# Performance work log

Hardware: AMD Instinct MI355X
Metric: run time of the kernel (lower is better)

## Reference

```python
import jax, jax.numpy as jnp
import numpy as np

D_MODEL = 1024
D_FF = 2048
NUM_EXPERTS = 16
TOP_K = 2
CAPACITY_FACTOR = 1.25
BATCH, SEQ = 4, 2048


def setup_inputs() -> dict:
    key = jax.random.key(0)
    k0, k1, k2, k3 = jax.random.split(key, 4)
    x = jax.random.normal(k0, (BATCH, SEQ, D_MODEL), jnp.float32)
    gate_w = jax.random.normal(k1, (NUM_EXPERTS, D_MODEL), jnp.float32) / np.float32(np.sqrt(D_MODEL))
    w1 = jax.random.normal(k2, (NUM_EXPERTS, D_MODEL, D_FF), jnp.float32) / np.float32(np.sqrt(D_MODEL))
    w2 = jax.random.normal(k3, (NUM_EXPERTS, D_FF, D_MODEL), jnp.float32) / np.float32(np.sqrt(D_FF))
    return {"x": x, "gate_w": gate_w, "w1": w1, "w2": w2}


def reference(x, gate_w, w1, w2):
    B, S, d = x.shape
    T = B * S
    E, K = NUM_EXPERTS, TOP_K
    capacity = int(CAPACITY_FACTOR * T * K / E)  # static

    xf = x.reshape(T, d)                                  # [T, d]
    logits = xf @ gate_w.T                                # [T, E]
    probs = jax.nn.sigmoid(logits)
    top_vals, sel = jax.lax.top_k(probs, K)               # [T, K]
    weights = top_vals / (top_vals.sum(-1, keepdims=True) + 1e-6)

    # Capacity-based ranking: rank of each (token, slot) within its expert,
    # in flattened token-major order (matches torch cumsum over one-hot).
    flat_sel = sel.reshape(-1)                            # [T*K]
    onehot = jax.nn.one_hot(flat_sel, E, dtype=jnp.int32)
    ranks = jnp.take_along_axis(jnp.cumsum(onehot, axis=0), flat_sel[:, None], axis=1)[:, 0] - 1
    valid = ranks < capacity                              # [T*K]

    sentinel = E * capacity
    slot = jnp.where(valid, flat_sel * capacity + ranks, sentinel)

    # token-major repeat matches x_flat.unsqueeze(1).expand(-1,K,-1).reshape(-1,d)
    x_rep = jnp.repeat(xf, K, axis=0)                     # [T*K, d]
    padded = jnp.zeros((sentinel + 1, d), xf.dtype).at[slot].set(x_rep)
    padded = padded[:sentinel].reshape(E, capacity, d)    # [E, C, d]

    h = jax.nn.gelu(jnp.einsum('ecd,edf->ecf', padded, w1), approximate=False)
    out_padded = jnp.einsum('ecf,efd->ecd', h, w2).reshape(sentinel, d)

    gathered = out_padded[jnp.minimum(slot, sentinel - 1)]
    gathered = jnp.where(valid[:, None], gathered, jnp.zeros((), xf.dtype))
    out = (gathered * weights.reshape(-1)[:, None]).reshape(T, K, d).sum(axis=1)
    return out.reshape(B, S, d)
```

## Files before the change

kernel.cpp:

```cpp
#include <hip/hip_runtime.h>
#include <math.h>

#define T_TOK 8192
#define DM 1024
#define DF 2048
#define NE 16
#define TK 2
#define CAP 1280

typedef __bf16 bf16x8 __attribute__((ext_vector_type(8)));
typedef float f32x4 __attribute__((ext_vector_type(4)));

__device__ __forceinline__ unsigned short f2bf(float f) {
  unsigned int u = __float_as_uint(f);
  unsigned int r = (u + 0x7fffu + ((u >> 16) & 1u)) >> 16;
  return (unsigned short)r;
}

__device__ __forceinline__ void async_copy16(const void* g, void* l) {
  __builtin_amdgcn_global_load_lds(
      (const __attribute__((address_space(1))) void*)g,
      (__attribute__((address_space(3))) void*)l, 16, 0, 0);
}

__global__ __launch_bounds__(256) void transpose_conv_kernel(
    const float* __restrict__ in, unsigned short* __restrict__ out, int R, int Cc) {
  __shared__ unsigned short tl[64][72];
  size_t eoff = (size_t)blockIdx.z * R * Cc;
  in += eoff; out += eoff;
  int c0 = blockIdx.x * 64, r0 = blockIdx.y * 64;
  int t = threadIdx.x;
#pragma unroll
  for (int i = 0; i < 4; i++) {
    int r = (t >> 4) + i * 16;
    int c = (t & 15) * 4;
    float4 v = *(const float4*)(in + (size_t)(r0 + r) * Cc + c0 + c);
    tl[c + 0][r] = f2bf(v.x);
    tl[c + 1][r] = f2bf(v.y);
    tl[c + 2][r] = f2bf(v.z);
    tl[c + 3][r] = f2bf(v.w);
  }
  __syncthreads();
#pragma unroll
  for (int i = 0; i < 2; i++) {
    int c = (t >> 3) + i * 32;
    int r = (t & 7) * 8;
    *(int4*)(out + (size_t)(c0 + c) * R + r0 + r) = *(const int4*)&tl[c][r];
  }
}

__global__ __launch_bounds__(256) void gate_kernel(
    const float* __restrict__ x, const float* __restrict__ gw,
    int* __restrict__ sel, float* __restrict__ wts) {
  __shared__ float sgw[NE * DM];
  int tid = threadIdx.x, lane = tid & 63, wv = tid >> 6;
  for (int i = tid; i < NE * DM / 4; i += 256)
    ((float4*)sgw)[i] = ((const float4*)gw)[i];
  __syncthreads();
  int t = blockIdx.x * 4 + wv;
  const float4* xr = (const float4*)(x + (size_t)t * DM);
  float4 xv[4];
#pragma unroll
  for (int j = 0; j < 4; j++) xv[j] = xr[j * 64 + lane];
  const float4* g4 = (const float4*)sgw;
  float acc[NE];
#pragma unroll
  for (int e = 0; e < NE; e++) {
    float s = 0.f;
#pragma unroll
    for (int j = 0; j < 4; j++) {
      float4 g = g4[e * 256 + j * 64 + lane];
      s += xv[j].x * g.x + xv[j].y * g.y + xv[j].z * g.z + xv[j].w * g.w;
    }
    acc[e] = s;
  }
#pragma unroll
  for (int e = 0; e < NE; e++) {
    float v = acc[e];
#pragma unroll
    for (int off = 32; off > 0; off >>= 1) v += __shfl_xor(v, off);
    acc[e] = v;
  }
  if (lane == 0) {
    float p[NE];
#pragma unroll
    for (int e = 0; e < NE; e++) p[e] = 1.f / (1.f + expf(-acc[e]));
    int i0 = 0;
#pragma unroll
    for (int e = 1; e < NE; e++) if (p[e] > p[i0]) i0 = e;
    int i1 = (i0 == 0) ? 1 : 0;
#pragma unroll
    for (int e = 0; e < NE; e++) if (e != i0 && p[e] > p[i1]) i1 = e;
    float v0 = p[i0], v1 = p[i1], s = v0 + v1 + 1e-6f;
    sel[2 * t] = i0; sel[2 * t + 1] = i1;
    wts[2 * t] = v0 / s; wts[2 * t + 1] = v1 / s;
  }
}

__global__ __launch_bounds__(256) void scan_kernel(
    const int* __restrict__ sel, int* __restrict__ exp_tok, int* __restrict__ counts) {
  int e = blockIdx.x;
  __shared__ int wsum[4];
  int tid = threadIdx.x, lane = tid & 63, wv = tid >> 6;
  int base = 0;
  for (int p0 = 0; p0 < T_TOK * TK; p0 += 256) {
    int p = p0 + tid;
    int flag = (sel[p] == e) ? 1 : 0;
    unsigned long long b = __ballot(flag);
    int pre = __popcll(b & ((1ull << lane) - 1ull));
    if (lane == 0) wsum[wv] = __popcll(b);
    __syncthreads();
    int wbase = 0;
#pragma unroll
    for (int i = 0; i < 4; i++) if (i < wv) wbase += wsum[i];
    int tot = wsum[0] + wsum[1] + wsum[2] + wsum[3];
    if (flag) {
      int rank = base + wbase + pre;
      if (rank < CAP) exp_tok[e * CAP + rank] = p;
    }
    base += tot;
    __syncthreads();
  }
  if (tid == 0) counts[e] = base < CAP ? base : CAP;
}

__global__ __launch_bounds__(128) void gather_kernel(
    const float* __restrict__ x, const int* __restrict__ exp_tok,
    const int* __restrict__ counts, unsigned short* __restrict__ Xp) {
  int i = blockIdx.x, e = blockIdx.y;
  int tid = threadIdx.x;
  unsigned short* dst = Xp + ((size_t)e * CAP + i) * DM;
  int4 pk = make_int4(0, 0, 0, 0);
  if (i < counts[e]) {
    int p = exp_tok[e * CAP + i];
    int t = p >> 1;
    const float4* src = (const float4*)(x + (size_t)t * DM);
    float4 v0 = src[tid * 2];
    float4 v1 = src[tid * 2 + 1];
    union { unsigned short u[8]; int4 v; } q;
    q.u[0] = f2bf(v0.x); q.u[1] = f2bf(v0.y); q.u[2] = f2bf(v0.z); q.u[3] = f2bf(v0.w);
    q.u[4] = f2bf(v1.x); q.u[5] = f2bf(v1.y); q.u[6] = f2bf(v1.z); q.u[7] = f2bf(v1.w);
    pk = q.v;
  }
  ((int4*)dst)[tid] = pk;
}

__global__ __launch_bounds__(256) void gemm1_kernel(
    const unsigned short* __restrict__ A, const unsigned short* __restrict__ Bt,
    unsigned short* __restrict__ C, int M, int N, int K,
    size_t sA, size_t sB, size_t sC) {
  __shared__ unsigned short As[128 * 32];
  __shared__ unsigned short Bs[128 * 32];
  A += (size_t)blockIdx.z * sA;
  Bt += (size_t)blockIdx.z * sB;
  C += (size_t)blockIdx.z * sC;
  int m0 = blockIdx.y * 128, n0 = blockIdx.x * 128;
  int tid = threadIdx.x;
  int lane = tid & 63;
  int wv = tid >> 6;
  int wm = (wv >> 1) * 64, wn = (wv & 1) * 64;
  int qd = lane >> 4, lm = lane & 15;
  int sa = (lm >> 1) & 3;
  int chunk = (tid & 3) ^ ((tid >> 3) & 3);

  const unsigned short* a0 = A + (size_t)(m0 + (tid >> 2)) * K + chunk * 8;
  const unsigned short* a1 = a0 + (size_t)64 * K;
  const unsigned short* b0 = Bt + (size_t)(n0 + (tid >> 2)) * K + chunk * 8;
  const unsigned short* b1 = b0 + (size_t)64 * K;
  char* lAs = (char*)As;
  char* lBs = (char*)Bs;

  f32x4 acc[4][4] = {};
  for (int k0 = 0; k0 < K; k0 += 32) {
    __syncthreads();
    async_copy16(a0 + k0, lAs + tid * 16);
    async_copy16(a1 + k0, lAs + (tid + 256) * 16);
    async_copy16(b0 + k0, lBs + tid * 16);
    async_copy16(b1 + k0, lBs + (tid + 256) * 16);
    __syncthreads();
    bf16x8 af[4], bfr[4];
#pragma unroll
    for (int i = 0; i < 4; i++)
      af[i] = *(const bf16x8*)(lAs + (wm + i * 16 + lm) * 64 + (qd ^ sa) * 16);
#pragma unroll
    for (int j = 0; j < 4; j++)
      bfr[j] = *(const bf16x8*)(lBs + (wn + j * 16 + lm) * 64 + (qd ^ sa) * 16);
#pragma unroll
    for (int i = 0; i < 4; i++)
#pragma unroll
      for (int j = 0; j < 4; j++)
        acc[i][j] = __builtin_amdgcn_mfma_f32_16x16x32_bf16(af[i], bfr[j], acc[i][j], 0, 0, 0);
  }
#pragma unroll
  for (int i = 0; i < 4; i++) {
    int row = m0 + wm + i * 16 + qd * 4;
#pragma unroll
    for (int j = 0; j < 4; j++) {
      int col = n0 + wn + j * 16 + lm;
#pragma unroll
      for (int r = 0; r < 4; r++) {
        float v = acc[i][j][r];
        v = 0.5f * v * (1.f + erff(v * 0.70710678118f));
        C[(size_t)(row + r) * N + col] = f2bf(v);
      }
    }
  }
}

__global__ __launch_bounds__(256) void gemm2_kernel(
    const unsigned short* __restrict__ A, const unsigned short* __restrict__ Bt,
    float* __restrict__ out, const int* __restrict__ exp_tok,
    const int* __restrict__ counts, const float* __restrict__ wts,
    int M, int N, int K, size_t sA, size_t sB) {
  __shared__ unsigned short As[128 * 32];
  __shared__ unsigned short Bs[128 * 32];
  int e = blockIdx.z;
  A += (size_t)e * sA;
  Bt += (size_t)e * sB;
  int m0 = blockIdx.y * 128, n0 = blockIdx.x * 128;
  int tid = threadIdx.x;
  int lane = tid & 63;
  int wv = tid >> 6;
  int wm = (wv >> 1) * 64, wn = (wv & 1) * 64;
  int qd = lane >> 4, lm = lane & 15;
  int sa = (lm >> 1) & 3;
  int chunk = (tid & 3) ^ ((tid >> 3) & 3);

  const unsigned short* a0 = A + (size_t)(m0 + (tid >> 2)) * K + chunk * 8;
  const unsigned short* a1 = a0 + (size_t)64 * K;
  const unsigned short* b0 = Bt + (size_t)(n0 + (tid >> 2)) * K + chunk * 8;
  const unsigned short* b1 = b0 + (size_t)64 * K;
  char* lAs = (char*)As;
  char* lBs = (char*)Bs;

  f32x4 acc[4][4] = {};
  for (int k0 = 0; k0 < K; k0 += 32) {
    __syncthreads();
    async_copy16(a0 + k0, lAs + tid * 16);
    async_copy16(a1 + k0, lAs + (tid + 256) * 16);
    async_copy16(b0 + k0, lBs + tid * 16);
    async_copy16(b1 + k0, lBs + (tid + 256) * 16);
    __syncthreads();
    bf16x8 af[4], bfr[4];
#pragma unroll
    for (int i = 0; i < 4; i++)
      af[i] = *(const bf16x8*)(lAs + (wm + i * 16 + lm) * 64 + (qd ^ sa) * 16);
#pragma unroll
    for (int j = 0; j < 4; j++)
      bfr[j] = *(const bf16x8*)(lBs + (wn + j * 16 + lm) * 64 + (qd ^ sa) * 16);
#pragma unroll
    for (int i = 0; i < 4; i++)
#pragma unroll
      for (int j = 0; j < 4; j++)
        acc[i][j] = __builtin_amdgcn_mfma_f32_16x16x32_bf16(af[i], bfr[j], acc[i][j], 0, 0, 0);
  }
  int cnt = counts[e];
#pragma unroll
  for (int i = 0; i < 4; i++) {
    int base_row = m0 + wm + i * 16 + qd * 4;
#pragma unroll
    for (int r = 0; r < 4; r++) {
      int slot = base_row + r;
      if (slot < cnt) {
        int p = exp_tok[e * CAP + slot];
        float w = wts[p];
        float* orow = out + (size_t)(p >> 1) * DM;
#pragma unroll
        for (int j = 0; j < 4; j++) {
          int col = n0 + wn + j * 16 + lm;
          atomicAdd(orow + col, w * acc[i][j][r]);
        }
      }
    }
  }
}

extern "C" void kernel_launch(void* const* d_in, const int* in_sizes, int n_in,
                              void* d_out, int out_size, void* d_ws, size_t ws_size,
                              hipStream_t stream) {
  (void)in_sizes; (void)n_in; (void)out_size; (void)ws_size;
  const float* x  = (const float*)d_in[0];
  const float* gw = (const float*)d_in[1];
  const float* w1 = (const float*)d_in[2];
  const float* w2 = (const float*)d_in[3];
  float* out = (float*)d_out;

  char* ws = (char*)d_ws;
  unsigned short* w1t = (unsigned short*)ws; ws += (size_t)NE * DM * DF * 2;
  unsigned short* w2t = (unsigned short*)ws; ws += (size_t)NE * DF * DM * 2;
  unsigned short* Xp  = (unsigned short*)ws; ws += (size_t)NE * CAP * DM * 2;
  unsigned short* H   = (unsigned short*)ws; ws += (size_t)NE * CAP * DF * 2;
  int* sel = (int*)ws;       ws += (size_t)T_TOK * TK * 4;
  float* wts = (float*)ws;   ws += (size_t)T_TOK * TK * 4;
  int* exp_tok = (int*)ws;   ws += (size_t)NE * CAP * 4;
  int* counts = (int*)ws;    ws += (size_t)NE * 4;

  hipMemsetAsync(out, 0, (size_t)T_TOK * DM * 4, stream);

  transpose_conv_kernel<<<dim3(DF / 64, DM / 64, NE), 256, 0, stream>>>(w1, w1t, DM, DF);
  transpose_conv_kernel<<<dim3(DM / 64, DF / 64, NE), 256, 0, stream>>>(w2, w2t, DF, DM);
  gate_kernel<<<T_TOK / 4, 256, 0, stream>>>(x, gw, sel, wts);
  scan_kernel<<<NE, 256, 0, stream>>>(sel, exp_tok, counts);
  gather_kernel<<<dim3(CAP, NE), 128, 0, stream>>>(x, exp_tok, counts, Xp);
  gemm1_kernel<<<dim3(DF / 128, CAP / 128, NE), 256, 0, stream>>>(
      Xp, w1t, H, CAP, DF, DM, (size_t)CAP * DM, (size_t)DM * DF, (size_t)CAP * DF);
  gemm2_kernel<<<dim3(DM / 128, CAP / 128, NE), 256, 0, stream>>>(
      H, w2t, out, exp_tok, counts, wts, CAP, DM, DF, (size_t)CAP * DF, (size_t)DF * DM);
}
```

Measured before the change: 747.9 us.

## Replace atomic scatter with bf16 expert outputs and per-token combine kernel

```diff
diff --git a/kernel.cpp b/kernel.cpp
--- a/kernel.cpp
+++ b/kernel.cpp
@@ -15,6 +15,10 @@
   unsigned int u = __float_as_uint(f);
   unsigned int r = (u + 0x7fffu + ((u >> 16) & 1u)) >> 16;
   return (unsigned short)r;
+}
+
+__device__ __forceinline__ float bf2f(unsigned short u) {
+  return __uint_as_float((unsigned int)u << 16);
 }
 
 __device__ __forceinline__ void async_copy16(const void* g, void* l) {
@@ -57,71 +61,88 @@
   for (int i = tid; i < NE * DM / 4; i += 256)
     ((float4*)sgw)[i] = ((const float4*)gw)[i];
   __syncthreads();
-  int t = blockIdx.x * 4 + wv;
-  const float4* xr = (const float4*)(x + (size_t)t * DM);
-  float4 xv[4];
-#pragma unroll
-  for (int j = 0; j < 4; j++) xv[j] = xr[j * 64 + lane];
   const float4* g4 = (const float4*)sgw;
-  float acc[NE];
-#pragma unroll
-  for (int e = 0; e < NE; e++) {
-    float s = 0.f;
-#pragma unroll
-    for (int j = 0; j < 4; j++) {
-      float4 g = g4[e * 256 + j * 64 + lane];
-      s += xv[j].x * g.x + xv[j].y * g.y + xv[j].z * g.z + xv[j].w * g.w;
-    }
-    acc[e] = s;
-  }
-#pragma unroll
-  for (int e = 0; e < NE; e++) {
-    float v = acc[e];
-#pragma unroll
-    for (int off = 32; off > 0; off >>= 1) v += __shfl_xor(v, off);
-    acc[e] = v;
-  }
-  if (lane == 0) {
-    float p[NE];
-#pragma unroll
-    for (int e = 0; e < NE; e++) p[e] = 1.f / (1.f + expf(-acc[e]));
-    int i0 = 0;
-#pragma unroll
-    for (int e = 1; e < NE; e++) if (p[e] > p[i0]) i0 = e;
-    int i1 = (i0 == 0) ? 1 : 0;
-#pragma unroll
-    for (int e = 0; e < NE; e++) if (e != i0 && p[e] > p[i1]) i1 = e;
-    float v0 = p[i0], v1 = p[i1], s = v0 + v1 + 1e-6f;
-    sel[2 * t] = i0; sel[2 * t + 1] = i1;
-    wts[2 * t] = v0 / s; wts[2 * t + 1] = v1 / s;
-  }
-}
-
-__global__ __launch_bounds__(256) void scan_kernel(
-    const int* __restrict__ sel, int* __restrict__ exp_tok, int* __restrict__ counts) {
+  for (int it = 0; it < 16; it++) {
+    int t = blockIdx.x * 64 + wv * 16 + it;
+    const float4* xr = (const float4*)(x + (size_t)t * DM);
+    float4 xv[4];
+#pragma unroll
+    for (int j = 0; j < 4; j++) xv[j] = xr[j * 64 + lane];
+    float acc[NE];
+#pragma unroll
+    for (int e = 0; e < NE; e++) {
+      float s = 0.f;
+#pragma unroll
+      for (int j = 0; j < 4; j++) {
+        float4 g = g4[e * 256 + j * 64 + lane];
+        s += xv[j].x * g.x + xv[j].y * g.y + xv[j].z * g.z + xv[j].w * g.w;
+      }
+      acc[e] = s;
+    }
+#pragma unroll
+    for (int e = 0; e < NE; e++) {
+      float v = acc[e];
+#pragma unroll
+      for (int off = 32; off > 0; off >>= 1) v += __shfl_xor(v, off);
+      acc[e] = v;
+    }
+    if (lane == 0) {
+      float p[NE];
+#pragma unroll
+      for (int e = 0; e < NE; e++) p[e] = 1.f / (1.f + expf(-acc[e]));
+      int i0 = 0;
+#pragma unroll
+      for (int e = 1; e < NE; e++) if (p[e] > p[i0]) i0 = e;
+      int i1 = (i0 == 0) ? 1 : 0;
+#pragma unroll
+      for (int e = 0; e < NE; e++) if (e != i0 && p[e] > p[i1]) i1 = e;
+      float v0 = p[i0], v1 = p[i1], s = v0 + v1 + 1e-6f;
+      sel[2 * t] = i0; sel[2 * t + 1] = i1;
+      wts[2 * t] = v0 / s; wts[2 * t + 1] = v1 / s;
+    }
+  }
+}
+
+__global__ __launch_bounds__(1024) void scan_kernel(
+    const int* __restrict__ sel, int* __restrict__ pos_slot,
+    int* __restrict__ exp_tok, int* __restrict__ counts) {
   int e = blockIdx.x;
-  __shared__ int wsum[4];
   int tid = threadIdx.x, lane = tid & 63, wv = tid >> 6;
-  int base = 0;
-  for (int p0 = 0; p0 < T_TOK * TK; p0 += 256) {
-    int p = p0 + tid;
-    int flag = (sel[p] == e) ? 1 : 0;
-    unsigned long long b = __ballot(flag);
-    int pre = __popcll(b & ((1ull << lane) - 1ull));
-    if (lane == 0) wsum[wv] = __popcll(b);
-    __syncthreads();
-    int wbase = 0;
-#pragma unroll
-    for (int i = 0; i < 4; i++) if (i < wv) wbase += wsum[i];
-    int tot = wsum[0] + wsum[1] + wsum[2] + wsum[3];
-    if (flag) {
-      int rank = base + wbase + pre;
-      if (rank < CAP) exp_tok[e * CAP + rank] = p;
-    }
-    base += tot;
-    __syncthreads();
-  }
-  if (tid == 0) counts[e] = base < CAP ? base : CAP;
+  __shared__ int wtot[16];
+  int local[16];
+  unsigned int flags = 0;
+  int run = 0;
+#pragma unroll
+  for (int it = 0; it < 16; it++) {
+    int p = wv * 1024 + it * 64 + lane;
+    int f = (sel[p] == e) ? 1 : 0;
+    unsigned long long b = __ballot(f);
+    if (f) { flags |= 1u << it; local[it] = run + __popcll(b & ((1ull << lane) - 1ull)); }
+    run += __popcll(b);
+  }
+  if (lane == 0) wtot[wv] = run;
+  __syncthreads();
+  int base = 0, total = 0;
+#pragma unroll
+  for (int i = 0; i < 16; i++) {
+    int v = wtot[i];
+    if (i < wv) base += v;
+    total += v;
+  }
+#pragma unroll
+  for (int it = 0; it < 16; it++) {
+    if (flags & (1u << it)) {
+      int p = wv * 1024 + it * 64 + lane;
+      int rank = base + local[it];
+      if (rank < CAP) {
+        pos_slot[p] = e * CAP + rank;
+        exp_tok[e * CAP + rank] = p;
+      } else {
+        pos_slot[p] = -1;
+      }
+    }
+  }
+  if (tid == 0) counts[e] = total < CAP ? total : CAP;
 }
 
 __global__ __launch_bounds__(128) void gather_kernel(
@@ -145,16 +166,21 @@
   ((int4*)dst)[tid] = pk;
 }
 
-__global__ __launch_bounds__(256) void gemm1_kernel(
+template <bool GELU>
+__global__ __launch_bounds__(256) void gemm_kernel(
     const unsigned short* __restrict__ A, const unsigned short* __restrict__ Bt,
-    unsigned short* __restrict__ C, int M, int N, int K,
-    size_t sA, size_t sB, size_t sC) {
+    unsigned short* __restrict__ C, const int* __restrict__ counts,
+    int N, int K, size_t sA, size_t sB, size_t sC) {
+  int e = blockIdx.z;
+  int m0 = blockIdx.y * 128;
+  int cnt = counts[e];
+  if (m0 >= cnt) return;
   __shared__ unsigned short As[128 * 32];
   __shared__ unsigned short Bs[128 * 32];
-  A += (size_t)blockIdx.z * sA;
-  Bt += (size_t)blockIdx.z * sB;
-  C += (size_t)blockIdx.z * sC;
-  int m0 = blockIdx.y * 128, n0 = blockIdx.x * 128;
+  A += (size_t)e * sA;
+  Bt += (size_t)e * sB;
+  C += (size_t)e * sC;
+  int n0 = blockIdx.x * 128;
   int tid = threadIdx.x;
   int lane = tid & 63;
   int wv = tid >> 6;
@@ -200,79 +226,33 @@
 #pragma unroll
       for (int r = 0; r < 4; r++) {
         float v = acc[i][j][r];
-        v = 0.5f * v * (1.f + erff(v * 0.70710678118f));
+        if (GELU) v = 0.5f * v * (1.f + erff(v * 0.70710678118f));
         C[(size_t)(row + r) * N + col] = f2bf(v);
       }
     }
   }
 }
 
-__global__ __launch_bounds__(256) void gemm2_kernel(
-    const unsigned short* __restrict__ A, const unsigned short* __restrict__ Bt,
-    float* __restrict__ out, const int* __restrict__ exp_tok,
-    const int* __restrict__ counts, const float* __restrict__ wts,
-    int M, int N, int K, size_t sA, size_t sB) {
-  __shared__ unsigned short As[128 * 32];
-  __shared__ unsigned short Bs[128 * 32];
-  int e = blockIdx.z;
-  A += (size_t)e * sA;
-  Bt += (size_t)e * sB;
-  int m0 = blockIdx.y * 128, n0 = blockIdx.x * 128;
-  int tid = threadIdx.x;
-  int lane = tid & 63;
-  int wv = tid >> 6;
-  int wm = (wv >> 1) * 64, wn = (wv & 1) * 64;
-  int qd = lane >> 4, lm = lane & 15;
-  int sa = (lm >> 1) & 3;
-  int chunk = (tid & 3) ^ ((tid >> 3) & 3);
-
-  const unsigned short* a0 = A + (size_t)(m0 + (tid >> 2)) * K + chunk * 8;
-  const unsigned short* a1 = a0 + (size_t)64 * K;
-  const unsigned short* b0 = Bt + (size_t)(n0 + (tid >> 2)) * K + chunk * 8;
-  const unsigned short* b1 = b0 + (size_t)64 * K;
-  char* lAs = (char*)As;
-  char* lBs = (char*)Bs;
-
-  f32x4 acc[4][4] = {};
-  for (int k0 = 0; k0 < K; k0 += 32) {
-    __syncthreads();
-    async_copy16(a0 + k0, lAs + tid * 16);
-    async_copy16(a1 + k0, lAs + (tid + 256) * 16);
-    async_copy16(b0 + k0, lBs + tid * 16);
-    async_copy16(b1 + k0, lBs + (tid + 256) * 16);
-    __syncthreads();
-    bf16x8 af[4], bfr[4];
-#pragma unroll
-    for (int i = 0; i < 4; i++)
-      af[i] = *(const bf16x8*)(lAs + (wm + i * 16 + lm) * 64 + (qd ^ sa) * 16);
-#pragma unroll
-    for (int j = 0; j < 4; j++)
-      bfr[j] = *(const bf16x8*)(lBs + (wn + j * 16 + lm) * 64 + (qd ^ sa) * 16);
-#pragma unroll
-    for (int i = 0; i < 4; i++)
-#pragma unroll
-      for (int j = 0; j < 4; j++)
-        acc[i][j] = __builtin_amdgcn_mfma_f32_16x16x32_bf16(af[i], bfr[j], acc[i][j], 0, 0, 0);
-  }
-  int cnt = counts[e];
-#pragma unroll
-  for (int i = 0; i < 4; i++) {
-    int base_row = m0 + wm + i * 16 + qd * 4;
-#pragma unroll
-    for (int r = 0; r < 4; r++) {
-      int slot = base_row + r;
-      if (slot < cnt) {
-        int p = exp_tok[e * CAP + slot];
-        float w = wts[p];
-        float* orow = out + (size_t)(p >> 1) * DM;
-#pragma unroll
-        for (int j = 0; j < 4; j++) {
-          int col = n0 + wn + j * 16 + lm;
-          atomicAdd(orow + col, w * acc[i][j][r]);
-        }
-      }
-    }
-  }
+__global__ __launch_bounds__(128) void combine_kernel(
+    const unsigned short* __restrict__ outp, const int* __restrict__ pos_slot,
+    const float* __restrict__ wts, float* __restrict__ out) {
+  int t = blockIdx.x, tid = threadIdx.x;
+  float acc[8] = {0.f, 0.f, 0.f, 0.f, 0.f, 0.f, 0.f, 0.f};
+#pragma unroll
+  for (int k = 0; k < 2; k++) {
+    int p = 2 * t + k;
+    int s = pos_slot[p];
+    if (s >= 0) {
+      float w = wts[p];
+      union { int4 v; unsigned short u[8]; } q;
+      q.v = *(const int4*)(outp + (size_t)s * DM + tid * 8);
+#pragma unroll
+      for (int i = 0; i < 8; i++) acc[i] += w * bf2f(q.u[i]);
+    }
+  }
+  float4* dst = (float4*)(out + (size_t)t * DM + tid * 8);
+  dst[0] = make_float4(acc[0], acc[1], acc[2], acc[3]);
+  dst[1] = make_float4(acc[4], acc[5], acc[6], acc[7]);
 }
 
 extern "C" void kernel_launch(void* const* d_in, const int* in_sizes, int n_in,
@@ -290,20 +270,21 @@
   unsigned short* w2t = (unsigned short*)ws; ws += (size_t)NE * DF * DM * 2;
   unsigned short* Xp  = (unsigned short*)ws; ws += (size_t)NE * CAP * DM * 2;
   unsigned short* H   = (unsigned short*)ws; ws += (size_t)NE * CAP * DF * 2;
+  unsigned short* outp = (unsigned short*)ws; ws += (size_t)NE * CAP * DM * 2;
   int* sel = (int*)ws;       ws += (size_t)T_TOK * TK * 4;
   float* wts = (float*)ws;   ws += (size_t)T_TOK * TK * 4;
+  int* pos_slot = (int*)ws;  ws += (size_t)T_TOK * TK * 4;
   int* exp_tok = (int*)ws;   ws += (size_t)NE * CAP * 4;
   int* counts = (int*)ws;    ws += (size_t)NE * 4;
 
-  hipMemsetAsync(out, 0, (size_t)T_TOK * DM * 4, stream);
-
   transpose_conv_kernel<<<dim3(DF / 64, DM / 64, NE), 256, 0, stream>>>(w1, w1t, DM, DF);
   transpose_conv_kernel<<<dim3(DM / 64, DF / 64, NE), 256, 0, stream>>>(w2, w2t, DF, DM);
-  gate_kernel<<<T_TOK / 4, 256, 0, stream>>>(x, gw, sel, wts);
-  scan_kernel<<<NE, 256, 0, stream>>>(sel, exp_tok, counts);
+  gate_kernel<<<T_TOK / 64, 256, 0, stream>>>(x, gw, sel, wts);
+  scan_kernel<<<NE, 1024, 0, stream>>>(sel, pos_slot, exp_tok, counts);
   gather_kernel<<<dim3(CAP, NE), 128, 0, stream>>>(x, exp_tok, counts, Xp);
-  gemm1_kernel<<<dim3(DF / 128, CAP / 128, NE), 256, 0, stream>>>(
-      Xp, w1t, H, CAP, DF, DM, (size_t)CAP * DM, (size_t)DM * DF, (size_t)CAP * DF);
-  gemm2_kernel<<<dim3(DM / 128, CAP / 128, NE), 256, 0, stream>>>(
-      H, w2t, out, exp_tok, counts, wts, CAP, DM, DF, (size_t)CAP * DF, (size_t)DF * DM);
-}
+  gemm_kernel<true><<<dim3(DF / 128, CAP / 128, NE), 256, 0, stream>>>(
+      Xp, w1t, H, counts, DF, DM, (size_t)CAP * DM, (size_t)DM * DF, (size_t)CAP * DF);
+  gemm_kernel<false><<<dim3(DM / 128, CAP / 128, NE), 256, 0, stream>>>(
+      H, w2t, outp, counts, DM, DF, (size_t)CAP * DF, (size_t)DF * DM, (size_t)CAP * DM);
+  combine_kernel<<<T_TOK, 128, 0, stream>>>(outp, pos_slot, wts, out);
+}
```

After: 763.5 us. 1.02x slower.
